# Kernel tuning notes

Hardware: AMD Instinct MI355X
Metric: run time of the kernel (lower is better)

## Reference

```python
import jax, jax.numpy as jnp
import numpy as np

B, N, D, K = 8, 8192, 256, 3


def setup_inputs() -> dict:
    key = jax.random.key(0)
    k0, k1, k2, k3 = jax.random.split(key, 4)
    basic_units = jax.random.normal(k0, (B, N, D), dtype=jnp.float32)
    # learned params: offset/modulation linear weights (K, D) and conv weight (D, D, K)
    offset_w = jax.random.normal(k1, (K, D), dtype=jnp.float32) * 0.02
    mod_w = jax.random.normal(k2, (K, D), dtype=jnp.float32) * 0.1
    fan_in = D * K
    weight = jax.random.normal(k3, (D, D, K), dtype=jnp.float32) * np.sqrt(2.0 / fan_in)
    return {"basic_units": basic_units, "offset_w": offset_w, "mod_w": mod_w, "weight": weight}


def reference(basic_units, offset_w, mod_w, weight):
    b, n, d = basic_units.shape
    k = weight.shape[2]
    # offsets and modulation per token per kernel tap: (B, N, K)
    offset = jnp.einsum('bnd,kd->bnk', basic_units, offset_w)
    modulation = jax.nn.sigmoid(jnp.einsum('bnd,kd->bnk', basic_units, mod_w))
    # base sampling position i + k - K//2, perturbed by data-dependent offset
    base = (jnp.arange(n)[:, None] + jnp.arange(k)[None, :] - k // 2).astype(basic_units.dtype)  # (N, K)
    pos = base[None, :, :] + offset  # (B, N, K)
    valid = (pos >= 0) & (pos < n)
    floor_f = jnp.clip(jnp.floor(pos), 0, n - 1)
    fi = floor_f.astype(jnp.int32)               # (B, N, K)
    ci = jnp.minimum(fi + 1, n - 1)
    w_ceil = pos - floor_f
    w_floor = 1.0 - w_ceil

    def gather(idx):
        # x[b, idx[b, i, k], :] -> (B, N, K, D)
        return jnp.take_along_axis(basic_units, idx.reshape(b, n * k, 1), axis=1).reshape(b, n, k, d)

    interp = w_floor[..., None] * gather(fi) + w_ceil[..., None] * gather(ci)  # (B, N, K, D)
    # modulate, zero out-of-range taps, then per-tap matmul summed over taps
    modulated = interp * (modulation * valid.astype(interp.dtype))[..., None]
    out = jnp.einsum('dek,bike->bid', weight, modulated)
    return out
```

## Files before the change

### kernel.cpp

```cpp
#include <hip/hip_runtime.h>
#include <hip/hip_bf16.h>
#include <cstdint>


#define N_TOK 8192
#define DIM   256
#define KW    768
#define BM    64
#define BN    256
#define BK    32

typedef unsigned short u16;
typedef __attribute__((ext_vector_type(4))) float    floatx4;
typedef __attribute__((ext_vector_type(8))) __bf16   bf16x8;
typedef __attribute__((ext_vector_type(8))) u16      ushortx8;

__device__ __forceinline__ u16 f32_to_bf16_rne(float f) {
    uint32_t u = __float_as_uint(f);
    u += 0x7fffu + ((u >> 16) & 1u);
    return (u16)(u >> 16);
}

__global__ __launch_bounds__(256) void coef_kernel(
    const float* __restrict__ x, const float* __restrict__ offw,
    const float* __restrict__ modw, int4* __restrict__ coef)
{
    const int wave = threadIdx.x >> 6;
    const int lane = threadIdx.x & 63;
    const int t = blockIdx.x * 4 + wave;

    const float4 xv = ((const float4*)(x + (size_t)t * DIM))[lane];
    float s[6];
#pragma unroll
    for (int k = 0; k < 3; ++k) {
        float4 wv = ((const float4*)(offw + k * DIM))[lane];
        s[k]     = xv.x * wv.x + xv.y * wv.y + xv.z * wv.z + xv.w * wv.w;
        float4 mv = ((const float4*)(modw + k * DIM))[lane];
        s[3 + k] = xv.x * mv.x + xv.y * mv.y + xv.z * mv.z + xv.w * mv.w;
    }
#pragma unroll
    for (int d = 1; d < 64; d <<= 1) {
#pragma unroll
        for (int i = 0; i < 6; ++i) s[i] += __shfl_xor(s[i], d, 64);
    }
    if (lane < 3) {
        const int k = lane;
        const int n = t & (N_TOK - 1);
        float pos   = (float)(n + k - 1) + s[k];
        bool  valid = (pos >= 0.0f) && (pos < (float)N_TOK);
        float ff = floorf(pos);
        ff = fminf(fmaxf(ff, 0.0f), (float)(N_TOK - 1));
        int   fi = (int)ff;
        int   ci = min(fi + 1, N_TOK - 1);
        float wc = pos - ff;
        float m  = valid ? (1.0f / (1.0f + expf(-s[3 + k]))) : 0.0f;
        coef[t * 3 + k] = make_int4(fi, ci,
                                    __float_as_int((1.0f - wc) * m),
                                    __float_as_int(wc * m));
    }
}

__global__ __launch_bounds__(256) void packw_kernel(
    const float* __restrict__ W, u16* __restrict__ WB)
{
    const int d = blockIdx.x;
    const int e = threadIdx.x;
#pragma unroll
    for (int k = 0; k < 3; ++k)
        WB[d * KW + k * DIM + e] = f32_to_bf16_rne(W[d * KW + e * 3 + k]);
}

__global__ __launch_bounds__(512, 4) void deform_gemm_kernel(
    const float* __restrict__ x, const u16* __restrict__ WB,
    const int4* __restrict__ coef, float* __restrict__ out)
{
    __shared__ __align__(16) u16 As[2][BM * 40];
    __shared__ __align__(16) u16 Bs[2][BN * 40];

    const int tid  = threadIdx.x;
    const int wave = tid >> 6;
    const int lane = tid & 63;

    const int raw   = blockIdx.x;
    const int xcd   = raw & 7;
    const int lidx  = raw >> 3;
    const int mtile = xcd * 128 + lidx;
    const int t0 = mtile * BM;
    const float* xb = x + (size_t)(t0 / N_TOK) * N_TOK * DIM;

    const int tl  = tid >> 3;
    const int sub = tid & 7;
    const int br = tid >> 1;
    const int bh = tid & 1;

    const int wm = (wave & 1) * 32;
    const int wn = (wave >> 1) * 64;
    const int lrow = lane & 15;
    const int lq   = lane >> 4;

    const int4 cc0 = coef[(size_t)(t0 + tl) * 3 + 0];
    const int4 cc1 = coef[(size_t)(t0 + tl) * 3 + 1];
    const int4 cc2 = coef[(size_t)(t0 + tl) * 3 + 2];

    float4 pf, pc;
    uint4  pb0, pb1;
    float  wA, wC;

    auto loadg = [&](int kk) {
        const int tap = kk >> 3;
        const int4 c = (tap == 0) ? cc0 : (tap == 1 ? cc1 : cc2);
        const int e0 = (kk & 7) * 32 + sub * 4;
        wA = __int_as_float(c.z);
        wC = __int_as_float(c.w);
        pf = *(const float4*)(xb + (size_t)c.x * DIM + e0);
        pc = *(const float4*)(xb + (size_t)c.y * DIM + e0);
        const uint4* g = (const uint4*)(WB + (size_t)br * KW + kk * BK + bh * 16);
        pb0 = g[0];
        pb1 = g[1];
    };

    auto packstore = [&](int buf) {
        float r0 = wA * pf.x + wC * pc.x;
        float r1 = wA * pf.y + wC * pc.y;
        float r2 = wA * pf.z + wC * pc.z;
        float r3 = wA * pf.w + wC * pc.w;
        uint32_t p0 = __builtin_amdgcn_perm(__float_as_uint(r1), __float_as_uint(r0), 0x07060302u);
        uint32_t p1 = __builtin_amdgcn_perm(__float_as_uint(r3), __float_as_uint(r2), 0x07060302u);
        *(uint2*)&As[buf][tl * 40 + sub * 4] = make_uint2(p0, p1);
        uint4* bdst = (uint4*)&Bs[buf][br * 40 + bh * 16];
        bdst[0] = pb0;
        bdst[1] = pb1;
    };

    loadg(0);
    packstore(0);
    loadg(1);

    floatx4 acc[2][4];
#pragma unroll
    for (int i = 0; i < 2; ++i)
#pragma unroll
        for (int j = 0; j < 4; ++j) acc[i][j] = (floatx4){0.f, 0.f, 0.f, 0.f};

    __syncthreads();

    for (int kk = 0; kk < 24; ++kk) {
        const int cur = kk & 1;
        bf16x8 af[2], bfv[4];
#pragma unroll
        for (int i = 0; i < 2; ++i)
            af[i] = __builtin_bit_cast(bf16x8, *(const ushortx8*)&As[cur][(wm + i * 16 + lrow) * 40 + lq * 8]);
#pragma unroll
        for (int j = 0; j < 4; ++j)
            bfv[j] = __builtin_bit_cast(bf16x8, *(const ushortx8*)&Bs[cur][(wn + j * 16 + lrow) * 40 + lq * 8]);
        if (kk < 23) packstore(cur ^ 1);
        if (kk < 22) loadg(kk + 2);
#pragma unroll
        for (int i = 0; i < 2; ++i)
#pragma unroll
            for (int j = 0; j < 4; ++j)
                acc[i][j] = __builtin_amdgcn_mfma_f32_16x16x32_bf16(af[i], bfv[j], acc[i][j], 0, 0, 0);
        __syncthreads();
    }

#pragma unroll
    for (int i = 0; i < 2; ++i) {
#pragma unroll
        for (int r = 0; r < 4; ++r) {
            const int token = t0 + wm + i * 16 + lq * 4 + r;
            float* op = out + (size_t)token * DIM + wn + lrow;
#pragma unroll
            for (int j = 0; j < 4; ++j) op[j * 16] = acc[i][j][r];
        }
    }
}

extern "C" void kernel_launch(void* const* d_in, const int* in_sizes, int n_in,
                              void* d_out, int out_size, void* d_ws, size_t ws_size,
                              hipStream_t stream)
{
    const float* x    = (const float*)d_in[0];
    const float* offw = (const float*)d_in[1];
    const float* modw = (const float*)d_in[2];
    const float* W    = (const float*)d_in[3];
    float* out = (float*)d_out;

    const int tot_tok = 8 * N_TOK;
    int4* coef = (int4*)d_ws;
    u16*  WB   = (u16*)((char*)d_ws + (size_t)tot_tok * 3 * 16);

    coef_kernel<<<tot_tok / 4, 256, 0, stream>>>(x, offw, modw, coef);
    packw_kernel<<<DIM, 256, 0, stream>>>(W, WB);
    deform_gemm_kernel<<<tot_tok / BM, 512, 0, stream>>>(x, WB, coef, out);
}
```

Measured before the change: 176.8 us.

## Load weight fragments directly to registers and use 4-wave blocks with larger per-wave tiles

The GEMM block drops from 8 to 4 waves. Each wave now covers all 64 rows and 64 output columns, doubling the accumulators per wave. Weight (B) fragments are loaded straight from global memory into MFMA-ready registers with one-step prefetch, removing the shared-memory B buffer and its stores and reads. Each thread now gathers 8 elements instead of 4. This raises register pressure and puts B-fragment global loads directly on the MFMA feed path, relying on L2 and cache hits for weight reuse across blocks.

Result: slower. 205.9 us (+16.4%).

```diff
diff --git a/kernel.cpp b/kernel.cpp
--- a/kernel.cpp
+++ b/kernel.cpp
@@ -70,12 +70,11 @@
         WB[d * KW + k * DIM + e] = f32_to_bf16_rne(W[d * KW + e * 3 + k]);
 }
 
-__global__ __launch_bounds__(512, 4) void deform_gemm_kernel(
+__global__ __launch_bounds__(256, 3) void deform_gemm_kernel(
     const float* __restrict__ x, const u16* __restrict__ WB,
     const int4* __restrict__ coef, float* __restrict__ out)
 {
     __shared__ __align__(16) u16 As[2][BM * 40];
-    __shared__ __align__(16) u16 Bs[2][BN * 40];
 
     const int tid  = threadIdx.x;
     const int wave = tid >> 6;
@@ -88,13 +87,10 @@
     const int t0 = mtile * BM;
     const float* xb = x + (size_t)(t0 / N_TOK) * N_TOK * DIM;
 
-    const int tl  = tid >> 3;
-    const int sub = tid & 7;
-    const int br = tid >> 1;
-    const int bh = tid & 1;
-
-    const int wm = (wave & 1) * 32;
-    const int wn = (wave >> 1) * 64;
+    const int tl  = tid >> 2;
+    const int sub = tid & 3;
+
+    const int wn   = wave * 64;
     const int lrow = lane & 15;
     const int lq   = lane >> 4;
 
@@ -102,43 +98,58 @@
     const int4 cc1 = coef[(size_t)(t0 + tl) * 3 + 1];
     const int4 cc2 = coef[(size_t)(t0 + tl) * 3 + 2];
 
-    float4 pf, pc;
-    uint4  pb0, pb1;
+    const u16* bbase = WB + (size_t)(wn + lrow) * KW + lq * 8;
+
+    float4 pf0, pf1, pc0, pc1;
     float  wA, wC;
+    uint4  bn0, bn1, bn2, bn3;
+
+    auto loadB = [&](int kk) {
+        const u16* p = bbase + kk * BK;
+        bn0 = *(const uint4*)(p + 0 * 16 * KW);
+        bn1 = *(const uint4*)(p + 1 * 16 * KW);
+        bn2 = *(const uint4*)(p + 2 * 16 * KW);
+        bn3 = *(const uint4*)(p + 3 * 16 * KW);
+    };
 
     auto loadg = [&](int kk) {
         const int tap = kk >> 3;
         const int4 c = (tap == 0) ? cc0 : (tap == 1 ? cc1 : cc2);
-        const int e0 = (kk & 7) * 32 + sub * 4;
+        const int e0 = (kk & 7) * 32 + sub * 8;
         wA = __int_as_float(c.z);
         wC = __int_as_float(c.w);
-        pf = *(const float4*)(xb + (size_t)c.x * DIM + e0);
-        pc = *(const float4*)(xb + (size_t)c.y * DIM + e0);
-        const uint4* g = (const uint4*)(WB + (size_t)br * KW + kk * BK + bh * 16);
-        pb0 = g[0];
-        pb1 = g[1];
+        const float* rf = xb + (size_t)c.x * DIM + e0;
+        const float* rc = xb + (size_t)c.y * DIM + e0;
+        pf0 = *(const float4*)rf;
+        pf1 = *(const float4*)(rf + 4);
+        pc0 = *(const float4*)rc;
+        pc1 = *(const float4*)(rc + 4);
     };
 
     auto packstore = [&](int buf) {
-        float r0 = wA * pf.x + wC * pc.x;
-        float r1 = wA * pf.y + wC * pc.y;
-        float r2 = wA * pf.z + wC * pc.z;
-        float r3 = wA * pf.w + wC * pc.w;
+        float r0 = wA * pf0.x + wC * pc0.x;
+        float r1 = wA * pf0.y + wC * pc0.y;
+        float r2 = wA * pf0.z + wC * pc0.z;
+        float r3 = wA * pf0.w + wC * pc0.w;
+        float r4 = wA * pf1.x + wC * pc1.x;
+        float r5 = wA * pf1.y + wC * pc1.y;
+        float r6 = wA * pf1.z + wC * pc1.z;
+        float r7 = wA * pf1.w + wC * pc1.w;
         uint32_t p0 = __builtin_amdgcn_perm(__float_as_uint(r1), __float_as_uint(r0), 0x07060302u);
         uint32_t p1 = __builtin_amdgcn_perm(__float_as_uint(r3), __float_as_uint(r2), 0x07060302u);
-        *(uint2*)&As[buf][tl * 40 + sub * 4] = make_uint2(p0, p1);
-        uint4* bdst = (uint4*)&Bs[buf][br * 40 + bh * 16];
-        bdst[0] = pb0;
-        bdst[1] = pb1;
+        uint32_t p2 = __builtin_amdgcn_perm(__float_as_uint(r5), __float_as_uint(r4), 0x07060302u);
+        uint32_t p3 = __builtin_amdgcn_perm(__float_as_uint(r7), __float_as_uint(r6), 0x07060302u);
+        *(uint4*)&As[buf][tl * 40 + sub * 8] = make_uint4(p0, p1, p2, p3);
     };
 
     loadg(0);
     packstore(0);
     loadg(1);
-
-    floatx4 acc[2][4];
-#pragma unroll
-    for (int i = 0; i < 2; ++i)
+    loadB(0);
+
+    floatx4 acc[4][4];
+#pragma unroll
+    for (int i = 0; i < 4; ++i)
 #pragma unroll
         for (int j = 0; j < 4; ++j) acc[i][j] = (floatx4){0.f, 0.f, 0.f, 0.f};
 
@@ -146,28 +157,32 @@
 
     for (int kk = 0; kk < 24; ++kk) {
         const int cur = kk & 1;
-        bf16x8 af[2], bfv[4];
-#pragma unroll
-        for (int i = 0; i < 2; ++i)
-            af[i] = __builtin_bit_cast(bf16x8, *(const ushortx8*)&As[cur][(wm + i * 16 + lrow) * 40 + lq * 8]);
-#pragma unroll
-        for (int j = 0; j < 4; ++j)
-            bfv[j] = __builtin_bit_cast(bf16x8, *(const ushortx8*)&Bs[cur][(wn + j * 16 + lrow) * 40 + lq * 8]);
+        bf16x8 bf0 = __builtin_bit_cast(bf16x8, bn0);
+        bf16x8 bf1 = __builtin_bit_cast(bf16x8, bn1);
+        bf16x8 bf2 = __builtin_bit_cast(bf16x8, bn2);
+        bf16x8 bf3 = __builtin_bit_cast(bf16x8, bn3);
+        bf16x8 af[4];
+#pragma unroll
+        for (int i = 0; i < 4; ++i)
+            af[i] = __builtin_bit_cast(bf16x8, *(const ushortx8*)&As[cur][(i * 16 + lrow) * 40 + lq * 8]);
+        if (kk < 23) loadB(kk + 1);
         if (kk < 23) packstore(cur ^ 1);
         if (kk < 22) loadg(kk + 2);
 #pragma unroll
-        for (int i = 0; i < 2; ++i)
-#pragma unroll
-            for (int j = 0; j < 4; ++j)
-                acc[i][j] = __builtin_amdgcn_mfma_f32_16x16x32_bf16(af[i], bfv[j], acc[i][j], 0, 0, 0);
+        for (int i = 0; i < 4; ++i) {
+            acc[i][0] = __builtin_amdgcn_mfma_f32_16x16x32_bf16(af[i], bf0, acc[i][0], 0, 0, 0);
+            acc[i][1] = __builtin_amdgcn_mfma_f32_16x16x32_bf16(af[i], bf1, acc[i][1], 0, 0, 0);
+            acc[i][2] = __builtin_amdgcn_mfma_f32_16x16x32_bf16(af[i], bf2, acc[i][2], 0, 0, 0);
+            acc[i][3] = __builtin_amdgcn_mfma_f32_16x16x32_bf16(af[i], bf3, acc[i][3], 0, 0, 0);
+        }
         __syncthreads();
     }
 
 #pragma unroll
-    for (int i = 0; i < 2; ++i) {
+    for (int i = 0; i < 4; ++i) {
 #pragma unroll
         for (int r = 0; r < 4; ++r) {
-            const int token = t0 + wm + i * 16 + lq * 4 + r;
+            const int token = t0 + i * 16 + lq * 4 + r;
             float* op = out + (size_t)token * DIM + wn + lrow;
 #pragma unroll
             for (int j = 0; j < 4; ++j) op[j * 16] = acc[i][j][r];
@@ -191,5 +206,5 @@
 
     coef_kernel<<<tot_tok / 4, 256, 0, stream>>>(x, offw, modw, coef);
     packw_kernel<<<DIM, 256, 0, stream>>>(W, WB);
-    deform_gemm_kernel<<<tot_tok / BM, 512, 0, stream>>>(x, WB, coef, out);
-}
+    deform_gemm_kernel<<<tot_tok / BM, 256, 0, stream>>>(x, WB, coef, out);
+}
```

## Fuse coefficient computation into GEMM and load weights directly into registers

Applied to the files above, without the earlier changes.

Removes the separate coef kernel: each GEMM block now stages the offset and modulation weights in shared memory, computes the per-token dot products with 8-lane shuffle reductions, and derives the interpolation indices and weights in registers. The bf16 weight matrix is repacked into a tile-major layout so each wave can load its MFMA B fragments straight from global memory into registers, dropping the shared-memory B staging. This saves a kernel launch, the coef workspace round-trip, and LDS traffic for B. In exchange every block reloads B fragments from L2 on each K step, and there is extra prologue work and register pressure.

New measurement: 171.6 us. 2.9% less time.

```diff
diff --git a/kernel.cpp b/kernel.cpp
--- a/kernel.cpp
+++ b/kernel.cpp
@@ -21,61 +21,26 @@
     return (u16)(u >> 16);
 }
 
-__global__ __launch_bounds__(256) void coef_kernel(
-    const float* __restrict__ x, const float* __restrict__ offw,
-    const float* __restrict__ modw, int4* __restrict__ coef)
-{
-    const int wave = threadIdx.x >> 6;
-    const int lane = threadIdx.x & 63;
-    const int t = blockIdx.x * 4 + wave;
-
-    const float4 xv = ((const float4*)(x + (size_t)t * DIM))[lane];
-    float s[6];
-#pragma unroll
-    for (int k = 0; k < 3; ++k) {
-        float4 wv = ((const float4*)(offw + k * DIM))[lane];
-        s[k]     = xv.x * wv.x + xv.y * wv.y + xv.z * wv.z + xv.w * wv.w;
-        float4 mv = ((const float4*)(modw + k * DIM))[lane];
-        s[3 + k] = xv.x * mv.x + xv.y * mv.y + xv.z * mv.z + xv.w * mv.w;
-    }
-#pragma unroll
-    for (int d = 1; d < 64; d <<= 1) {
-#pragma unroll
-        for (int i = 0; i < 6; ++i) s[i] += __shfl_xor(s[i], d, 64);
-    }
-    if (lane < 3) {
-        const int k = lane;
-        const int n = t & (N_TOK - 1);
-        float pos   = (float)(n + k - 1) + s[k];
-        bool  valid = (pos >= 0.0f) && (pos < (float)N_TOK);
-        float ff = floorf(pos);
-        ff = fminf(fmaxf(ff, 0.0f), (float)(N_TOK - 1));
-        int   fi = (int)ff;
-        int   ci = min(fi + 1, N_TOK - 1);
-        float wc = pos - ff;
-        float m  = valid ? (1.0f / (1.0f + expf(-s[3 + k]))) : 0.0f;
-        coef[t * 3 + k] = make_int4(fi, ci,
-                                    __float_as_int((1.0f - wc) * m),
-                                    __float_as_int(wc * m));
-    }
-}
-
 __global__ __launch_bounds__(256) void packw_kernel(
-    const float* __restrict__ W, u16* __restrict__ WB)
+    const float* __restrict__ W, u16* __restrict__ WB2)
 {
     const int d = blockIdx.x;
     const int e = threadIdx.x;
 #pragma unroll
-    for (int k = 0; k < 3; ++k)
-        WB[d * KW + k * DIM + e] = f32_to_bf16_rne(W[d * KW + e * 3 + k]);
+    for (int k = 0; k < 3; ++k) {
+        const int kap = k * 256 + e;
+        WB2[((size_t)((kap >> 5) * 256 + d)) * 32 + (kap & 31)] =
+            f32_to_bf16_rne(W[d * KW + e * 3 + k]);
+    }
 }
 
 __global__ __launch_bounds__(512, 4) void deform_gemm_kernel(
-    const float* __restrict__ x, const u16* __restrict__ WB,
-    const int4* __restrict__ coef, float* __restrict__ out)
+    const float* __restrict__ x, const float* __restrict__ offw,
+    const float* __restrict__ modw, const u16* __restrict__ WB2,
+    float* __restrict__ out)
 {
-    __shared__ __align__(16) u16 As[2][BM * 40];
-    __shared__ __align__(16) u16 Bs[2][BN * 40];
+    __shared__ __align__(16) u16   As[2][BM * 40];
+    __shared__ __align__(16) float wlds[6 * DIM];
 
     const int tid  = threadIdx.x;
     const int wave = tid >> 6;
@@ -90,33 +55,82 @@
 
     const int tl  = tid >> 3;
     const int sub = tid & 7;
-    const int br = tid >> 1;
-    const int bh = tid & 1;
 
     const int wm = (wave & 1) * 32;
     const int wn = (wave >> 1) * 64;
     const int lrow = lane & 15;
     const int lq   = lane >> 4;
 
-    const int4 cc0 = coef[(size_t)(t0 + tl) * 3 + 0];
-    const int4 cc1 = coef[(size_t)(t0 + tl) * 3 + 1];
-    const int4 cc2 = coef[(size_t)(t0 + tl) * 3 + 2];
+    if (tid < 192)      ((float4*)wlds)[tid]       = ((const float4*)offw)[tid];
+    else if (tid < 384) ((float4*)wlds)[tid]       = ((const float4*)modw)[tid - 192];
+    __syncthreads();
+
+    float s[6];
+    {
+        const float* xr = x + (size_t)(t0 + tl) * DIM + sub * 32;
+        float4 xv[8];
+#pragma unroll
+        for (int i = 0; i < 8; ++i) xv[i] = ((const float4*)xr)[i];
+#pragma unroll
+        for (int w = 0; w < 6; ++w) {
+            const float4* wr = (const float4*)(wlds + w * DIM + sub * 32);
+            float a = 0.f;
+#pragma unroll
+            for (int i = 0; i < 8; ++i) {
+                float4 wv = wr[i];
+                a += xv[i].x * wv.x + xv[i].y * wv.y + xv[i].z * wv.z + xv[i].w * wv.w;
+            }
+            s[w] = a;
+        }
+    }
+#pragma unroll
+    for (int m = 1; m < 8; m <<= 1)
+#pragma unroll
+        for (int w = 0; w < 6; ++w) s[w] += __shfl_xor(s[w], m, 64);
+
+    int fi0, fi1, fi2, ci0, ci1, ci2;
+    float wa0, wa1, wa2, wc0, wc1, wc2;
+    {
+        const int n = (t0 + tl) & (N_TOK - 1);
+#pragma unroll
+        for (int k = 0; k < 3; ++k) {
+            float pos   = (float)(n + k - 1) + s[k];
+            bool  valid = (pos >= 0.0f) && (pos < (float)N_TOK);
+            float ff = floorf(pos);
+            ff = fminf(fmaxf(ff, 0.0f), (float)(N_TOK - 1));
+            int   fi = (int)ff;
+            int   ci = min(fi + 1, N_TOK - 1);
+            float wc = pos - ff;
+            float m  = valid ? (1.0f / (1.0f + expf(-s[3 + k]))) : 0.0f;
+            float wa = (1.0f - wc) * m;
+            float wcm = wc * m;
+            if (k == 0) { fi0 = fi; ci0 = ci; wa0 = wa; wc0 = wcm; }
+            if (k == 1) { fi1 = fi; ci1 = ci; wa1 = wa; wc1 = wcm; }
+            if (k == 2) { fi2 = fi; ci2 = ci; wa2 = wa; wc2 = wcm; }
+        }
+    }
 
     float4 pf, pc;
-    uint4  pb0, pb1;
     float  wA, wC;
+    uint4  bn0, bn1, bn2, bn3;
+
+    auto loadB = [&](int kk) {
+        const uint4* p = (const uint4*)(WB2 + ((size_t)(kk * 256 + wn + lrow)) * 32 + lq * 8);
+        bn0 = p[0];
+        bn1 = p[64];
+        bn2 = p[128];
+        bn3 = p[192];
+    };
 
     auto loadg = [&](int kk) {
         const int tap = kk >> 3;
-        const int4 c = (tap == 0) ? cc0 : (tap == 1 ? cc1 : cc2);
+        const int fi = (tap == 0) ? fi0 : (tap == 1 ? fi1 : fi2);
+        const int ci = (tap == 0) ? ci0 : (tap == 1 ? ci1 : ci2);
+        wA = (tap == 0) ? wa0 : (tap == 1 ? wa1 : wa2);
+        wC = (tap == 0) ? wc0 : (tap == 1 ? wc1 : wc2);
         const int e0 = (kk & 7) * 32 + sub * 4;
-        wA = __int_as_float(c.z);
-        wC = __int_as_float(c.w);
-        pf = *(const float4*)(xb + (size_t)c.x * DIM + e0);
-        pc = *(const float4*)(xb + (size_t)c.y * DIM + e0);
-        const uint4* g = (const uint4*)(WB + (size_t)br * KW + kk * BK + bh * 16);
-        pb0 = g[0];
-        pb1 = g[1];
+        pf = *(const float4*)(xb + (size_t)fi * DIM + e0);
+        pc = *(const float4*)(xb + (size_t)ci * DIM + e0);
     };
 
     auto packstore = [&](int buf) {
@@ -127,14 +141,12 @@
         uint32_t p0 = __builtin_amdgcn_perm(__float_as_uint(r1), __float_as_uint(r0), 0x07060302u);
         uint32_t p1 = __builtin_amdgcn_perm(__float_as_uint(r3), __float_as_uint(r2), 0x07060302u);
         *(uint2*)&As[buf][tl * 40 + sub * 4] = make_uint2(p0, p1);
-        uint4* bdst = (uint4*)&Bs[buf][br * 40 + bh * 16];
-        bdst[0] = pb0;
-        bdst[1] = pb1;
     };
 
     loadg(0);
     packstore(0);
     loadg(1);
+    loadB(0);
 
     floatx4 acc[2][4];
 #pragma unroll
@@ -146,20 +158,24 @@
 
     for (int kk = 0; kk < 24; ++kk) {
         const int cur = kk & 1;
-        bf16x8 af[2], bfv[4];
+        bf16x8 bf0 = __builtin_bit_cast(bf16x8, bn0);
+        bf16x8 bf1 = __builtin_bit_cast(bf16x8, bn1);
+        bf16x8 bf2 = __builtin_bit_cast(bf16x8, bn2);
+        bf16x8 bf3 = __builtin_bit_cast(bf16x8, bn3);
+        bf16x8 af[2];
 #pragma unroll
         for (int i = 0; i < 2; ++i)
             af[i] = __builtin_bit_cast(bf16x8, *(const ushortx8*)&As[cur][(wm + i * 16 + lrow) * 40 + lq * 8]);
-#pragma unroll
-        for (int j = 0; j < 4; ++j)
-            bfv[j] = __builtin_bit_cast(bf16x8, *(const ushortx8*)&Bs[cur][(wn + j * 16 + lrow) * 40 + lq * 8]);
+        if (kk < 23) loadB(kk + 1);
         if (kk < 23) packstore(cur ^ 1);
         if (kk < 22) loadg(kk + 2);
 #pragma unroll
-        for (int i = 0; i < 2; ++i)
-#pragma unroll
-            for (int j = 0; j < 4; ++j)
-                acc[i][j] = __builtin_amdgcn_mfma_f32_16x16x32_bf16(af[i], bfv[j], acc[i][j], 0, 0, 0);
+        for (int i = 0; i < 2; ++i) {
+            acc[i][0] = __builtin_amdgcn_mfma_f32_16x16x32_bf16(af[i], bf0, acc[i][0], 0, 0, 0);
+            acc[i][1] = __builtin_amdgcn_mfma_f32_16x16x32_bf16(af[i], bf1, acc[i][1], 0, 0, 0);
+            acc[i][2] = __builtin_amdgcn_mfma_f32_16x16x32_bf16(af[i], bf2, acc[i][2], 0, 0, 0);
+            acc[i][3] = __builtin_amdgcn_mfma_f32_16x16x32_bf16(af[i], bf3, acc[i][3], 0, 0, 0);
+        }
         __syncthreads();
     }
 
@@ -186,10 +202,8 @@
     float* out = (float*)d_out;
 
     const int tot_tok = 8 * N_TOK;
-    int4* coef = (int4*)d_ws;
-    u16*  WB   = (u16*)((char*)d_ws + (size_t)tot_tok * 3 * 16);
-
-    coef_kernel<<<tot_tok / 4, 256, 0, stream>>>(x, offw, modw, coef);
-    packw_kernel<<<DIM, 256, 0, stream>>>(W, WB);
-    deform_gemm_kernel<<<tot_tok / BM, 512, 0, stream>>>(x, WB, coef, out);
-}
+    u16* WB2 = (u16*)d_ws;
+
+    packw_kernel<<<DIM, 256, 0, stream>>>(W, WB2);
+    deform_gemm_kernel<<<tot_tok / BM, 512, 0, stream>>>(x, offw, modw, WB2, out);
+}
```
